# Optimization experiments

Hardware: AMD Instinct MI355X
Metric: run time of the kernel (lower is better)

## Reference

```python
import jax, jax.numpy as jnp
import numpy as np

HID, OUT = 128, 64
N_SOTU, N_TAXON = 500_000, 200_000
E_TT, E_TS, E_LBL = 200_000, 1_000_000, 500_000


def _sage(x_src, x_dst, src, dst, wl, bl, wr):
    """PyG SAGEConv (mean aggr): lin_l(mean of neighbor msgs) + lin_r(x_dst)."""
    n_dst = x_dst.shape[0]
    agg = jax.ops.segment_sum(x_src[src], dst, num_segments=n_dst)
    deg = jax.ops.segment_sum(jnp.ones(src.shape[0], x_src.dtype), dst, num_segments=n_dst)
    agg = agg / jnp.maximum(deg, 1.0)[:, None]
    return agg @ wl + bl + x_dst @ wr


def setup_inputs() -> dict:
    key = jax.random.key(0)
    ks = iter(jax.random.split(key, 40))

    def w(shape):
        fan_in = shape[0]
        return (jax.random.normal(next(ks), shape, jnp.float32) / np.sqrt(fan_in)).astype(jnp.float32)

    def ri(n, hi):
        return jax.random.randint(next(ks), (n,), 0, hi, dtype=jnp.int32)

    inp = {
        "sotu_ids": jnp.arange(N_SOTU, dtype=jnp.int32),
        "taxon_ids": jnp.arange(N_TAXON, dtype=jnp.int32),
        "ett_src": ri(E_TT, N_TAXON),
        "ett_dst": ri(E_TT, N_TAXON),
        "ets_src": ri(E_TS, N_TAXON),
        "ets_dst": ri(E_TS, N_SOTU),
        "elbl_row": ri(E_LBL, N_SOTU),
        "elbl_col": ri(E_LBL, N_TAXON),
        # embeddings
        "sotu_emb": jax.random.normal(next(ks), (N_SOTU, HID), jnp.float32),
        "taxon_emb": jax.random.normal(next(ks), (N_TAXON, HID), jnp.float32),
        # SOTU encoder: conv1 (taxon->taxon), conv2/3 (taxon->sotu), lin
        "s1_wl": w((HID, HID)), "s1_bl": jnp.zeros((HID,), jnp.float32), "s1_wr": w((HID, HID)),
        "s2_wl": w((HID, HID)), "s2_bl": jnp.zeros((HID,), jnp.float32), "s2_wr": w((HID, HID)),
        "s3_wl": w((HID, HID)), "s3_bl": jnp.zeros((HID,), jnp.float32), "s3_wr": w((HID, HID)),
        "sl_w": w((HID, OUT)), "sl_b": jnp.zeros((OUT,), jnp.float32),
        # Taxon encoder: conv1, conv2, lin
        "t1_wl": w((HID, HID)), "t1_bl": jnp.zeros((HID,), jnp.float32), "t1_wr": w((HID, HID)),
        "t2_wl": w((HID, HID)), "t2_bl": jnp.zeros((HID,), jnp.float32), "t2_wr": w((HID, HID)),
        "tl_w": w((HID, OUT)), "tl_b": jnp.zeros((OUT,), jnp.float32),
        # Edge decoder MLP
        "d1_w": w((2 * OUT, OUT)), "d1_b": jnp.zeros((OUT,), jnp.float32),
        "d2_w": w((OUT, 1)), "d2_b": jnp.zeros((1,), jnp.float32),
    }
    return inp


def reference(sotu_ids, taxon_ids, ett_src, ett_dst, ets_src, ets_dst,
              elbl_row, elbl_col, sotu_emb, taxon_emb,
              s1_wl, s1_bl, s1_wr, s2_wl, s2_bl, s2_wr, s3_wl, s3_bl, s3_wr,
              sl_w, sl_b, t1_wl, t1_bl, t1_wr, t2_wl, t2_bl, t2_wr, tl_w, tl_b,
              d1_w, d1_b, d2_w, d2_b):
    # embedding lookup
    x_sotu = sotu_emb[sotu_ids]          # [N_SOTU, HID]
    x_taxon = taxon_emb[taxon_ids]       # [N_TAXON, HID]
    # SOTU encoder
    taxon_x = jax.nn.relu(_sage(x_taxon, x_taxon, ett_src, ett_dst, s1_wl, s1_bl, s1_wr))
    sotu_x = jax.nn.relu(_sage(x_taxon, x_sotu, ets_src, ets_dst, s2_wl, s2_bl, s2_wr))
    sotu_x = jax.nn.relu(_sage(taxon_x, sotu_x, ets_src, ets_dst, s3_wl, s3_bl, s3_wr))
    z_sotu = sotu_x @ sl_w + sl_b        # [N_SOTU, OUT]
    # Taxon encoder
    tx = jax.nn.relu(_sage(x_taxon, x_taxon, ett_src, ett_dst, t1_wl, t1_bl, t1_wr))
    tx = jax.nn.relu(_sage(tx, tx, ett_src, ett_dst, t2_wl, t2_bl, t2_wr))
    z_taxon = tx @ tl_w + tl_b           # [N_TAXON, OUT]
    # Edge decoder: gather endpoints, fused MLP
    z = jnp.concatenate([z_sotu[elbl_row], z_taxon[elbl_col]], axis=-1)  # [E_LBL, 2*OUT]
    h = jax.nn.relu(z @ d1_w + d1_b)
    return (h @ d2_w + d2_b).reshape(-1)  # [E_LBL]
```

## Files before the change

kernel.cpp:

```cpp
#include <hip/hip_runtime.h>

#define HID 128
#define OUTD 64
#define N_SOTU 500000
#define N_TAXON 200000
#define E_TT 200000
#define E_TS 1000000
#define E_LBL 500000
#define SCAN_TILE 2048

typedef short s16x8 __attribute__((ext_vector_type(8)));
typedef float f32x4 __attribute__((ext_vector_type(4)));

__device__ __forceinline__ unsigned short f2bf(float f) {
    unsigned u = __builtin_bit_cast(unsigned, f);
    u += 0x7FFFu + ((u >> 16) & 1u);
    return (unsigned short)(u >> 16);
}
__device__ __forceinline__ float bf2f(unsigned short h) {
    unsigned u = ((unsigned)h) << 16;
    return __builtin_bit_cast(float, u);
}

__global__ void hist_kernel(const int* __restrict__ dst, int n, int* __restrict__ rp) {
    int e = blockIdx.x * 256 + threadIdx.x;
    if (e < n) atomicAdd(&rp[dst[e]], 1);
}

__global__ __launch_bounds__(256) void scan1_kernel(int* __restrict__ a, int n, int* __restrict__ bsums) {
    __shared__ int tsum[256];
    const int t = threadIdx.x;
    const int base = blockIdx.x * SCAN_TILE + t * 8;
    int v[8]; int s = 0;
#pragma unroll
    for (int i = 0; i < 8; i++) {
        int x = (base + i < n) ? a[base + i] : 0;
        s += x; v[i] = s;
    }
    tsum[t] = s;
    __syncthreads();
    for (int off = 1; off < 256; off <<= 1) {
        int x = (t >= off) ? tsum[t - off] : 0;
        __syncthreads();
        tsum[t] += x;
        __syncthreads();
    }
    const int prev = (t > 0) ? tsum[t - 1] : 0;
#pragma unroll
    for (int i = 0; i < 8; i++)
        if (base + i < n) a[base + i] = v[i] + prev;
    if (t == 255) bsums[blockIdx.x] = tsum[255];
}

__global__ __launch_bounds__(256) void scan2_kernel(int* __restrict__ bsums, int nb) {
    __shared__ int tsum[256];
    const int t = threadIdx.x;
    tsum[t] = (t < nb) ? bsums[t] : 0;
    __syncthreads();
    for (int off = 1; off < 256; off <<= 1) {
        int x = (t >= off) ? tsum[t - off] : 0;
        __syncthreads();
        tsum[t] += x;
        __syncthreads();
    }
    if (t < nb) bsums[t] = tsum[t];
}

__global__ __launch_bounds__(256) void scan3_kernel(int* __restrict__ a, int n, const int* __restrict__ bsums) {
    const int b = blockIdx.x;
    if (b == 0) return;
    const int add = bsums[b - 1];
    const int base = b * SCAN_TILE + threadIdx.x * 8;
#pragma unroll
    for (int i = 0; i < 8; i++)
        if (base + i < n) a[base + i] += add;
}

__global__ void fill_kernel(const int* __restrict__ src, const int* __restrict__ dst, int n,
                            int* __restrict__ rp, int* __restrict__ sl) {
    int e = blockIdx.x * 256 + threadIdx.x;
    if (e < n) {
        int pos = atomicSub(&rp[dst[e]], 1) - 1;
        sl[pos] = src[e];
    }
}

__global__ __launch_bounds__(256) void cvt_kernel(
    int n_rows, const float* __restrict__ xf, const int* __restrict__ ids,
    unsigned short* __restrict__ o)
{
    int idx = blockIdx.x * 256 + threadIdx.x;
    if (idx >= n_rows * 16) return;
    int r = idx >> 4, l = idx & 15;
    int s = ids ? ids[r] : r;
    const float* p = xf + (size_t)s * HID + l * 8;
    float4 v0 = *(const float4*)p;
    float4 v1 = *(const float4*)(p + 4);
    s16x8 ov;
    ov[0] = (short)f2bf(v0.x); ov[1] = (short)f2bf(v0.y);
    ov[2] = (short)f2bf(v0.z); ov[3] = (short)f2bf(v0.w);
    ov[4] = (short)f2bf(v1.x); ov[5] = (short)f2bf(v1.y);
    ov[6] = (short)f2bf(v1.z); ov[7] = (short)f2bf(v1.w);
    *(s16x8*)(o + (size_t)r * HID + l * 8) = ov;
}

__device__ __forceinline__ int wt_idx(int n, int k) {
    return n * 256 + ((((k >> 3) ^ n) & 31) << 3) + (k & 7);
}

__global__ __launch_bounds__(256) void fsage_kernel(
    int n_rows, int row0,
    const unsigned short* __restrict__ gsrc,
    const int* __restrict__ rp, const int* __restrict__ sl,
    int n_dst_total, int n_edges,
    const float* __restrict__ xf, const unsigned short* __restrict__ xb,
    const int* __restrict__ xids,
    const float* __restrict__ wl, const float* __restrict__ wr,
    const float* __restrict__ bl,
    unsigned short* __restrict__ out)
{
    __shared__ __align__(16) unsigned short WT[128 * 256];
    __shared__ __align__(16) unsigned short AGG[4][16 * 128];
    for (int idx = threadIdx.x; idx < 128 * 128; idx += 256) {
        int n = idx & 127, k = idx >> 7;
        WT[wt_idx(n, k)]       = f2bf(wl[idx]);
        WT[wt_idx(n, k + 128)] = f2bf(wr[idx]);
    }
    __syncthreads();
    const int lane = threadIdx.x & 63, wid = threadIdx.x >> 6;
    const int l16 = lane & 15, q = lane >> 4;
    const int n_tiles = n_rows >> 4;
    const int stride = gridDim.x * 4;
    for (int tile = blockIdx.x * 4 + wid; tile < n_tiles; tile += stride) {
        const int base = tile << 4;
#pragma unroll
        for (int it = 0; it < 4; ++it) {
            const int lr = it * 4 + q;
            const int d = row0 + base + lr;
            const int start = rp[d];
            const int end = (d + 1 < n_dst_total) ? rp[d + 1] : n_edges;
            float acc[8] = {0.f, 0.f, 0.f, 0.f, 0.f, 0.f, 0.f, 0.f};
            for (int j = start; j < end; ++j) {
                const int s = sl[j];
                s16x8 b = *(const s16x8*)(gsrc + (size_t)s * HID + l16 * 8);
#pragma unroll
                for (int i = 0; i < 8; i++) acc[i] += bf2f((unsigned short)b[i]);
            }
            const float inv = (end > start) ? 1.0f / (float)(end - start) : 0.0f;
            s16x8 o;
#pragma unroll
            for (int i = 0; i < 8; i++) o[i] = (short)f2bf(acc[i] * inv);
            *(s16x8*)&AGG[wid][lr * 128 + ((l16 * 8) ^ ((lr & 7) << 3))] = o;
        }
        asm volatile("s_waitcnt lgkmcnt(0)" ::: "memory");
        const int lrow = base + l16;
        const size_t xrow = xids ? (size_t)xids[lrow] : (size_t)(row0 + lrow);
        f32x4 acc[8] = {};
#pragma unroll
        for (int ks = 0; ks < 4; ks++) {
            const int cu = ks * 32 + q * 8;
            s16x8 a = *(const s16x8*)&AGG[wid][l16 * 128 + (cu ^ ((l16 & 7) << 3))];
#pragma unroll
            for (int nt = 0; nt < 8; nt++) {
                s16x8 b = *(const s16x8*)&WT[wt_idx(nt * 16 + l16, cu)];
                acc[nt] = __builtin_amdgcn_mfma_f32_16x16x32_bf16(a, b, acc[nt], 0, 0, 0);
            }
        }
#pragma unroll
        for (int ks = 0; ks < 4; ks++) {
            s16x8 a;
            if (xf) {
                const float* xp = xf + xrow * HID + ks * 32 + q * 8;
                float4 v0 = *(const float4*)xp;
                float4 v1 = *(const float4*)(xp + 4);
                a[0] = (short)f2bf(v0.x); a[1] = (short)f2bf(v0.y);
                a[2] = (short)f2bf(v0.z); a[3] = (short)f2bf(v0.w);
                a[4] = (short)f2bf(v1.x); a[5] = (short)f2bf(v1.y);
                a[6] = (short)f2bf(v1.z); a[7] = (short)f2bf(v1.w);
            } else {
                a = *(const s16x8*)(xb + xrow * HID + ks * 32 + q * 8);
            }
            const int kb = 128 + ks * 32 + q * 8;
#pragma unroll
            for (int nt = 0; nt < 8; nt++) {
                s16x8 b = *(const s16x8*)&WT[wt_idx(nt * 16 + l16, kb)];
                acc[nt] = __builtin_amdgcn_mfma_f32_16x16x32_bf16(a, b, acc[nt], 0, 0, 0);
            }
        }
#pragma unroll
        for (int nt = 0; nt < 8; nt++) {
            const int n = nt * 16 + l16;
            const float bv = bl[n];
#pragma unroll
            for (int i = 0; i < 4; i++) {
                float v = acc[nt][i] + bv;
                out[(size_t)(base + q * 4 + i) * HID + n] = f2bf(fmaxf(v, 0.0f));
            }
        }
    }
}

__global__ __launch_bounds__(256) void proj_kernel(
    int n_nodes, const unsigned short* __restrict__ x,
    const float* __restrict__ w, const float* __restrict__ bias, unsigned short* __restrict__ z)
{
    const int lane = threadIdx.x & 63, wid = threadIdx.x >> 6;
    const int l16 = lane & 15, q = lane >> 4;
    s16x8 bfr[4][4];
#pragma unroll
    for (int ks = 0; ks < 4; ks++)
#pragma unroll
        for (int nt = 0; nt < 4; nt++)
#pragma unroll
            for (int i = 0; i < 8; i++)
                bfr[ks][nt][i] = (short)f2bf(w[(ks * 32 + q * 8 + i) * OUTD + nt * 16 + l16]);
    const int n_tiles = n_nodes >> 4;
    const int stride = gridDim.x * 4;
    for (int tile = blockIdx.x * 4 + wid; tile < n_tiles; tile += stride) {
        const int base = tile << 4;
        const size_t mrow = (size_t)(base + l16);
        f32x4 acc[4] = {};
#pragma unroll
        for (int ks = 0; ks < 4; ks++) {
            s16x8 a = *(const s16x8*)(x + mrow * HID + ks * 32 + q * 8);
#pragma unroll
            for (int nt = 0; nt < 4; nt++)
                acc[nt] = __builtin_amdgcn_mfma_f32_16x16x32_bf16(a, bfr[ks][nt], acc[nt], 0, 0, 0);
        }
#pragma unroll
        for (int nt = 0; nt < 4; nt++) {
            const int n = nt * 16 + l16;
            const float bv = bias[n];
#pragma unroll
            for (int i = 0; i < 4; i++)
                z[(size_t)(base + q * 4 + i) * OUTD + n] = f2bf(acc[nt][i] + bv);
        }
    }
}

__global__ __launch_bounds__(256) void dec_kernel(
    const int* __restrict__ erow, const int* __restrict__ ecol,
    const unsigned short* __restrict__ zs, const unsigned short* __restrict__ zt,
    const float* __restrict__ w1, const float* __restrict__ b1,
    const float* __restrict__ w2, const float* __restrict__ b2,
    float* __restrict__ out)
{
    const int lane = threadIdx.x & 63, wid = threadIdx.x >> 6;
    const int l16 = lane & 15, q = lane >> 4;
    s16x8 bfr[4][4];
#pragma unroll
    for (int ks = 0; ks < 4; ks++)
#pragma unroll
        for (int nt = 0; nt < 4; nt++)
#pragma unroll
            for (int i = 0; i < 8; i++)
                bfr[ks][nt][i] = (short)f2bf(w1[(ks * 32 + q * 8 + i) * OUTD + nt * 16 + l16]);
    float b1v[4], w2v[4];
#pragma unroll
    for (int nt = 0; nt < 4; nt++) {
        b1v[nt] = b1[nt * 16 + l16];
        w2v[nt] = w2[nt * 16 + l16];
    }
    const float b2v = b2[0];
    const int n_tiles = E_LBL >> 4;
    for (int tile = blockIdx.x * 4 + wid; tile < n_tiles; tile += gridDim.x * 4) {
        const int em = tile * 16 + l16;
        const size_t r = (size_t)erow[em], c = (size_t)ecol[em];
        f32x4 acc[4] = {};
        s16x8 a0 = *(const s16x8*)(zs + r * OUTD + q * 8);
        s16x8 a1 = *(const s16x8*)(zs + r * OUTD + 32 + q * 8);
        s16x8 a2 = *(const s16x8*)(zt + c * OUTD + q * 8);
        s16x8 a3 = *(const s16x8*)(zt + c * OUTD + 32 + q * 8);
#pragma unroll
        for (int nt = 0; nt < 4; nt++) {
            acc[nt] = __builtin_amdgcn_mfma_f32_16x16x32_bf16(a0, bfr[0][nt], acc[nt], 0, 0, 0);
            acc[nt] = __builtin_amdgcn_mfma_f32_16x16x32_bf16(a1, bfr[1][nt], acc[nt], 0, 0, 0);
            acc[nt] = __builtin_amdgcn_mfma_f32_16x16x32_bf16(a2, bfr[2][nt], acc[nt], 0, 0, 0);
            acc[nt] = __builtin_amdgcn_mfma_f32_16x16x32_bf16(a3, bfr[3][nt], acc[nt], 0, 0, 0);
        }
        float s[4] = {0.0f, 0.0f, 0.0f, 0.0f};
#pragma unroll
        for (int nt = 0; nt < 4; nt++)
#pragma unroll
            for (int i = 0; i < 4; i++)
                s[i] += fmaxf(acc[nt][i] + b1v[nt], 0.0f) * w2v[nt];
#pragma unroll
        for (int off = 8; off >= 1; off >>= 1)
#pragma unroll
            for (int i = 0; i < 4; i++)
                s[i] += __shfl_down(s[i], off, 16);
        if (l16 == 0) {
#pragma unroll
            for (int i = 0; i < 4; i++)
                out[tile * 16 + q * 4 + i] = s[i] + b2v;
        }
    }
}

static void build_csr(const int* src, const int* dst, int n_edges, int n_dst,
                      int* rp, int* sl, int* bsums, hipStream_t stream) {
    hipMemsetAsync(rp, 0, (size_t)n_dst * 4, stream);
    hist_kernel<<<(n_edges + 255) / 256, 256, 0, stream>>>(dst, n_edges, rp);
    const int nb = (n_dst + SCAN_TILE - 1) / SCAN_TILE;
    scan1_kernel<<<nb, 256, 0, stream>>>(rp, n_dst, bsums);
    scan2_kernel<<<1, 256, 0, stream>>>(bsums, nb);
    scan3_kernel<<<nb, 256, 0, stream>>>(rp, n_dst, bsums);
    fill_kernel<<<(n_edges + 255) / 256, 256, 0, stream>>>(src, dst, n_edges, rp, sl);
}

extern "C" void kernel_launch(void* const* d_in, const int* in_sizes, int n_in,
                              void* d_out, int out_size, void* d_ws, size_t ws_size,
                              hipStream_t stream) {
    (void)in_sizes; (void)n_in; (void)out_size; (void)ws_size;
    const int* sotu_ids  = (const int*)d_in[0];
    const int* taxon_ids = (const int*)d_in[1];
    const int* ett_src   = (const int*)d_in[2];
    const int* ett_dst   = (const int*)d_in[3];
    const int* ets_src   = (const int*)d_in[4];
    const int* ets_dst   = (const int*)d_in[5];
    const int* elbl_row  = (const int*)d_in[6];
    const int* elbl_col  = (const int*)d_in[7];
    const float* sotu_emb  = (const float*)d_in[8];
    const float* taxon_emb = (const float*)d_in[9];
    const float* s1_wl = (const float*)d_in[10]; const float* s1_bl = (const float*)d_in[11]; const float* s1_wr = (const float*)d_in[12];
    const float* s2_wl = (const float*)d_in[13]; const float* s2_bl = (const float*)d_in[14]; const float* s2_wr = (const float*)d_in[15];
    const float* s3_wl = (const float*)d_in[16]; const float* s3_bl = (const float*)d_in[17]; const float* s3_wr = (const float*)d_in[18];
    const float* sl_w  = (const float*)d_in[19]; const float* sl_b  = (const float*)d_in[20];
    const float* t1_wl = (const float*)d_in[21]; const float* t1_bl = (const float*)d_in[22]; const float* t1_wr = (const float*)d_in[23];
    const float* t2_wl = (const float*)d_in[24]; const float* t2_bl = (const float*)d_in[25]; const float* t2_wr = (const float*)d_in[26];
    const float* tl_w  = (const float*)d_in[27]; const float* tl_b  = (const float*)d_in[28];
    const float* d1_w  = (const float*)d_in[29]; const float* d1_b  = (const float*)d_in[30];
    const float* d2_w  = (const float*)d_in[31]; const float* d2_b  = (const float*)d_in[32];
    float* out = (float*)d_out;

    char* ws = (char*)d_ws;
    size_t off = 0;
    auto alloc = [&](size_t bytes) { void* p = ws + off; off = (off + bytes + 255) & ~(size_t)255; return p; };
    unsigned short* tb      = (unsigned short*)alloc((size_t)N_TAXON * HID * 2);
    unsigned short* taxon_x = (unsigned short*)alloc((size_t)N_TAXON * HID * 2);
    unsigned short* tx1     = (unsigned short*)alloc((size_t)N_TAXON * HID * 2);
    unsigned short* tx2     = (unsigned short*)alloc((size_t)N_TAXON * HID * 2);
    unsigned short* sotu_x  = (unsigned short*)alloc((size_t)N_SOTU * HID * 2);
    unsigned short* z_taxon = (unsigned short*)alloc((size_t)N_TAXON * OUTD * 2);
    int* rp_ts = (int*)alloc((size_t)N_SOTU * 4);
    int* sl_ts = (int*)alloc((size_t)E_TS * 4);
    int* rp_tt = (int*)alloc((size_t)N_TAXON * 4);
    int* sl_tt = (int*)alloc((size_t)E_TT * 4);
    int* bsums = (int*)alloc(256 * 4);
    unsigned short* z_sotu = tx1;

    build_csr(ett_src, ett_dst, E_TT, N_TAXON, rp_tt, sl_tt, bsums, stream);
    build_csr(ets_src, ets_dst, E_TS, N_SOTU, rp_ts, sl_ts, bsums, stream);

    cvt_kernel<<<(N_TAXON * 16 + 255) / 256, 256, 0, stream>>>(N_TAXON, taxon_emb, taxon_ids, tb);

    fsage_kernel<<<512, 256, 0, stream>>>(N_TAXON, 0, tb, rp_tt, sl_tt, N_TAXON, E_TT,
                                          nullptr, tb, nullptr, s1_wl, s1_wr, s1_bl, taxon_x);
    fsage_kernel<<<512, 256, 0, stream>>>(N_TAXON, 0, tb, rp_tt, sl_tt, N_TAXON, E_TT,
                                          nullptr, tb, nullptr, t1_wl, t1_wr, t1_bl, tx1);

    fsage_kernel<<<512, 256, 0, stream>>>(N_TAXON, 0, tx1, rp_tt, sl_tt, N_TAXON, E_TT,
                                          nullptr, tx1, nullptr, t2_wl, t2_wr, t2_bl, tx2);
    proj_kernel<<<1024, 256, 0, stream>>>(N_TAXON, tx2, tl_w, tl_b, z_taxon);

    fsage_kernel<<<512, 256, 0, stream>>>(N_SOTU, 0, tb, rp_ts, sl_ts, N_SOTU, E_TS,
                                          sotu_emb, nullptr, sotu_ids, s2_wl, s2_wr, s2_bl, sotu_x);
    fsage_kernel<<<512, 256, 0, stream>>>(N_SOTU, 0, taxon_x, rp_ts, sl_ts, N_SOTU, E_TS,
                                          nullptr, sotu_x, nullptr, s3_wl, s3_wr, s3_bl, sotu_x);
    proj_kernel<<<1024, 256, 0, stream>>>(N_SOTU, sotu_x, sl_w, sl_b, z_sotu);

    dec_kernel<<<1024, 256, 0, stream>>>(elbl_row, elbl_col, z_sotu, z_taxon,
                                         d1_w, d1_b, d2_w, d2_b, out);
}
```

Measured before the change: 1.495 ms.

## Batch neighbor gathers and prefetch root features in fused SAGE kernel

The fused SAGE kernel now issues the first four neighbor-row gathers for all four rows of a tile up front, masked by degree weights, before accumulating. It also loads the root-node features at the start of the tile so their latency overlaps with aggregation. The goal is more memory-level parallelism, replacing a serial dependent-gather loop for low-degree nodes. The trade-off is higher register pressure, which launch_bounds(256,2) constrains and may cause spills. Rows with zero edges now issue redundant loads.

```diff
diff --git a/kernel.cpp b/kernel.cpp
--- a/kernel.cpp
+++ b/kernel.cpp
@@ -108,7 +108,7 @@
     return n * 256 + ((((k >> 3) ^ n) & 31) << 3) + (k & 7);
 }
 
-__global__ __launch_bounds__(256) void fsage_kernel(
+__global__ __launch_bounds__(256, 2) void fsage_kernel(
     int n_rows, int row0,
     const unsigned short* __restrict__ gsrc,
     const int* __restrict__ rp, const int* __restrict__ sl,
@@ -133,29 +133,89 @@
     const int stride = gridDim.x * 4;
     for (int tile = blockIdx.x * 4 + wid; tile < n_tiles; tile += stride) {
         const int base = tile << 4;
+        const int lrow = base + l16;
+        const size_t xrow = xids ? (size_t)xids[lrow] : (size_t)(row0 + lrow);
+        float4 xv[8];
+        s16x8 axb[4];
+        if (xf) {
+            const float* xp = xf + xrow * HID + q * 8;
+#pragma unroll
+            for (int ks = 0; ks < 4; ++ks) {
+                xv[ks * 2]     = *(const float4*)(xp + ks * 32);
+                xv[ks * 2 + 1] = *(const float4*)(xp + ks * 32 + 4);
+            }
+        } else {
+            const unsigned short* xp = xb + xrow * HID + q * 8;
+#pragma unroll
+            for (int ks = 0; ks < 4; ++ks) axb[ks] = *(const s16x8*)(xp + ks * 32);
+        }
+        int st[4], cc[4];
+        s16x8 r[4][4];
+        float wgt[4][4];
 #pragma unroll
         for (int it = 0; it < 4; ++it) {
             const int lr = it * 4 + q;
             const int d = row0 + base + lr;
-            const int start = rp[d];
-            const int end = (d + 1 < n_dst_total) ? rp[d + 1] : n_edges;
-            float acc[8] = {0.f, 0.f, 0.f, 0.f, 0.f, 0.f, 0.f, 0.f};
-            for (int j = start; j < end; ++j) {
-                const int s = sl[j];
-                s16x8 b = *(const s16x8*)(gsrc + (size_t)s * HID + l16 * 8);
-#pragma unroll
-                for (int i = 0; i < 8; i++) acc[i] += bf2f((unsigned short)b[i]);
-            }
-            const float inv = (end > start) ? 1.0f / (float)(end - start) : 0.0f;
+            const int s_ = rp[d];
+            const int e_ = (d + 1 < n_dst_total) ? rp[d + 1] : n_edges;
+            st[it] = s_;
+            const int c = e_ - s_;
+            cc[it] = c;
+            const int js = (s_ < n_edges) ? s_ : (n_edges - 1);
+            const int i1 = (c > 1) ? s_ + 1 : js;
+            const int i2 = (c > 2) ? s_ + 2 : js;
+            const int i3 = (c > 3) ? s_ + 3 : js;
+            const int s0 = sl[js], s1 = sl[i1], s2 = sl[i2], s3 = sl[i3];
+            r[it][0] = *(const s16x8*)(gsrc + (size_t)s0 * HID + l16 * 8);
+            r[it][1] = *(const s16x8*)(gsrc + (size_t)s1 * HID + l16 * 8);
+            r[it][2] = *(const s16x8*)(gsrc + (size_t)s2 * HID + l16 * 8);
+            r[it][3] = *(const s16x8*)(gsrc + (size_t)s3 * HID + l16 * 8);
+            wgt[it][0] = (c > 0) ? 1.0f : 0.0f;
+            wgt[it][1] = (c > 1) ? 1.0f : 0.0f;
+            wgt[it][2] = (c > 2) ? 1.0f : 0.0f;
+            wgt[it][3] = (c > 3) ? 1.0f : 0.0f;
+        }
+#pragma unroll
+        for (int it = 0; it < 4; ++it) {
+            float acc[8];
+#pragma unroll
+            for (int i = 0; i < 8; i++)
+                acc[i] = wgt[it][0] * bf2f((unsigned short)r[it][0][i])
+                       + wgt[it][1] * bf2f((unsigned short)r[it][1][i])
+                       + wgt[it][2] * bf2f((unsigned short)r[it][2][i])
+                       + wgt[it][3] * bf2f((unsigned short)r[it][3][i]);
+            if (cc[it] > 4) {
+                const int e_ = st[it] + cc[it];
+                for (int j = st[it] + 4; j < e_; ++j) {
+                    const int s = sl[j];
+                    s16x8 b = *(const s16x8*)(gsrc + (size_t)s * HID + l16 * 8);
+#pragma unroll
+                    for (int i = 0; i < 8; i++) acc[i] += bf2f((unsigned short)b[i]);
+                }
+            }
+            const float inv = (cc[it] > 0) ? 1.0f / (float)cc[it] : 0.0f;
+            const int lr = it * 4 + q;
             s16x8 o;
 #pragma unroll
             for (int i = 0; i < 8; i++) o[i] = (short)f2bf(acc[i] * inv);
             *(s16x8*)&AGG[wid][lr * 128 + ((l16 * 8) ^ ((lr & 7) << 3))] = o;
         }
         asm volatile("s_waitcnt lgkmcnt(0)" ::: "memory");
-        const int lrow = base + l16;
-        const size_t xrow = xids ? (size_t)xids[lrow] : (size_t)(row0 + lrow);
-        f32x4 acc[8] = {};
+        s16x8 ax[4];
+        if (xf) {
+#pragma unroll
+            for (int ks = 0; ks < 4; ++ks) {
+                float4 v0 = xv[ks * 2], v1 = xv[ks * 2 + 1];
+                ax[ks][0] = (short)f2bf(v0.x); ax[ks][1] = (short)f2bf(v0.y);
+                ax[ks][2] = (short)f2bf(v0.z); ax[ks][3] = (short)f2bf(v0.w);
+                ax[ks][4] = (short)f2bf(v1.x); ax[ks][5] = (short)f2bf(v1.y);
+                ax[ks][6] = (short)f2bf(v1.z); ax[ks][7] = (short)f2bf(v1.w);
+            }
+        } else {
+#pragma unroll
+            for (int ks = 0; ks < 4; ++ks) ax[ks] = axb[ks];
+        }
+        f32x4 acc4[8] = {};
 #pragma unroll
         for (int ks = 0; ks < 4; ks++) {
             const int cu = ks * 32 + q * 8;
@@ -163,28 +223,16 @@
 #pragma unroll
             for (int nt = 0; nt < 8; nt++) {
                 s16x8 b = *(const s16x8*)&WT[wt_idx(nt * 16 + l16, cu)];
-                acc[nt] = __builtin_amdgcn_mfma_f32_16x16x32_bf16(a, b, acc[nt], 0, 0, 0);
+                acc4[nt] = __builtin_amdgcn_mfma_f32_16x16x32_bf16(a, b, acc4[nt], 0, 0, 0);
             }
         }
 #pragma unroll
         for (int ks = 0; ks < 4; ks++) {
-            s16x8 a;
-            if (xf) {
-                const float* xp = xf + xrow * HID + ks * 32 + q * 8;
-                float4 v0 = *(const float4*)xp;
-                float4 v1 = *(const float4*)(xp + 4);
-                a[0] = (short)f2bf(v0.x); a[1] = (short)f2bf(v0.y);
-                a[2] = (short)f2bf(v0.z); a[3] = (short)f2bf(v0.w);
-                a[4] = (short)f2bf(v1.x); a[5] = (short)f2bf(v1.y);
-                a[6] = (short)f2bf(v1.z); a[7] = (short)f2bf(v1.w);
-            } else {
-                a = *(const s16x8*)(xb + xrow * HID + ks * 32 + q * 8);
-            }
             const int kb = 128 + ks * 32 + q * 8;
 #pragma unroll
             for (int nt = 0; nt < 8; nt++) {
                 s16x8 b = *(const s16x8*)&WT[wt_idx(nt * 16 + l16, kb)];
-                acc[nt] = __builtin_amdgcn_mfma_f32_16x16x32_bf16(a, b, acc[nt], 0, 0, 0);
+                acc4[nt] = __builtin_amdgcn_mfma_f32_16x16x32_bf16(ax[ks], b, acc4[nt], 0, 0, 0);
             }
         }
 #pragma unroll
@@ -193,7 +241,7 @@
             const float bv = bl[n];
 #pragma unroll
             for (int i = 0; i < 4; i++) {
-                float v = acc[nt][i] + bv;
+                float v = acc4[nt][i] + bv;
                 out[(size_t)(base + q * 4 + i) * HID + n] = f2bf(fmaxf(v, 0.0f));
             }
         }
```

Result: faster. 1.341 ms (-10.3%).
